# Optimization experiments

Hardware: AMD Instinct MI355X
Metric: run time of the kernel (lower is better)

Reference implementation:

```python
import jax, jax.numpy as jnp
import numpy as np

N_NODES = 50000
N_EDGES = 800000
IN_CH = 128
HID = 64
OUT_CH = 40


def _sage_conv(x, src, dst, W_l, b_l, W_r):
    # PyG SAGEConv (mean aggr): out = lin_l(mean_{j in N(i)} x_j) + lin_r(x_i)
    msgs = x[src]                                                # [E, d]
    summed = jax.ops.segment_sum(msgs, dst, num_segments=N_NODES)
    counts = jax.ops.segment_sum(jnp.ones((src.shape[0],), x.dtype), dst,
                                 num_segments=N_NODES)
    mean = summed / jnp.maximum(counts, 1.0)[:, None]            # [N, d]
    return mean @ W_l.T + b_l + x @ W_r.T


def setup_inputs() -> dict:
    key = jax.random.key(0)
    ks = jax.random.split(key, 8)
    x = jax.random.normal(ks[0], (N_NODES, IN_CH), dtype=jnp.float32)
    edge_index = jax.random.randint(ks[1], (2, N_EDGES), 0, N_NODES, dtype=jnp.int64)
    s1 = 1.0 / np.sqrt(IN_CH)
    s2 = 1.0 / np.sqrt(HID)
    W1_l = jax.random.uniform(ks[2], (HID, IN_CH), jnp.float32, -s1, s1)
    W1_r = jax.random.uniform(ks[3], (HID, IN_CH), jnp.float32, -s1, s1)
    b1 = jax.random.uniform(ks[4], (HID,), jnp.float32, -s1, s1)
    W2_l = jax.random.uniform(ks[5], (OUT_CH, HID), jnp.float32, -s2, s2)
    W2_r = jax.random.uniform(ks[6], (OUT_CH, HID), jnp.float32, -s2, s2)
    b2 = jax.random.uniform(ks[7], (OUT_CH,), jnp.float32, -s2, s2)
    return {"x": x, "edge_index": edge_index, "W1_l": W1_l, "b1": b1,
            "W1_r": W1_r, "W2_l": W2_l, "b2": b2, "W2_r": W2_r}


def reference(x, edge_index, W1_l, b1, W1_r, W2_l, b2, W2_r):
    src, dst = edge_index[0], edge_index[1]
    h = _sage_conv(x, src, dst, W1_l, b1, W1_r)
    h = jax.nn.relu(h)                       # dropout is identity in eval
    h = _sage_conv(h, src, dst, W2_l, b2, W2_r)
    return jax.nn.log_softmax(h, axis=-1)
```

## Files before the change

kernel.cpp:

```cpp
#include <hip/hip_runtime.h>

#define N_NODES 50000
#define N_EDGES 800000
#define IN_CH 128
#define HID 64
#define OUT_CH 40
#define BSHIFT 7
#define BNODES 128
#define NBUCKETS 391
#define NBLK 256
#define EPB 3125
#define NSEG (NBUCKETS * NBLK)
#define SCHUNK 1024
#define NSCANA ((NSEG + SCHUNK - 1) / SCHUNK)
#define MAXB 4096
#define NXBLK 782


typedef __attribute__((ext_vector_type(8))) short short8v;
typedef __attribute__((ext_vector_type(4))) float float4v;

__device__ __forceinline__ unsigned f2bf_u(float f) {
  unsigned u = __float_as_uint(f);
  return (u + 0x7FFF + ((u >> 16) & 1)) >> 16;
}
__device__ __forceinline__ ushort f2bf(float f) { return (ushort)f2bf_u(f); }
__device__ __forceinline__ float bf2f(ushort u) {
  return __uint_as_float(((unsigned)u) << 16);
}
__device__ __forceinline__ float bflo(unsigned u) {
  return __uint_as_float(u << 16);
}
__device__ __forceinline__ float bfhi(unsigned u) {
  return __uint_as_float(u & 0xFFFF0000u);
}

__device__ __forceinline__ uint4 pack8(const float* p) {
  float4 a = *reinterpret_cast<const float4*>(p);
  float4 b = *reinterpret_cast<const float4*>(p + 4);
  uint4 r;
  r.x = f2bf_u(a.x) | (f2bf_u(a.y) << 16);
  r.y = f2bf_u(a.z) | (f2bf_u(a.w) << 16);
  r.z = f2bf_u(b.x) | (f2bf_u(b.y) << 16);
  r.w = f2bf_u(b.z) | (f2bf_u(b.w) << 16);
  return r;
}

__global__ __launch_bounds__(256) void histX_kernel(
    const int* __restrict__ dst, int* __restrict__ blkcnt,
    const float* __restrict__ x, const float* __restrict__ W1l,
    const float* __restrict__ W1r, const float* __restrict__ b1,
    ushort* __restrict__ xwl, float* __restrict__ xwr) {
  __shared__ int h[NBUCKETS];
  __shared__ ushort sWl[64 * 128];
  __shared__ ushort sWr[64 * 128];
  __shared__ ushort sx[64 * 128];
  __shared__ float sb[64];

  if (blockIdx.x < NBLK) {
    for (int i = threadIdx.x; i < NBUCKETS; i += 256) h[i] = 0;
    __syncthreads();
    int blk = blockIdx.x;
    int e0 = blk * EPB, e1 = min(e0 + EPB, N_EDGES);
    for (int e = e0 + threadIdx.x; e < e1; e += 256)
      atomicAdd(&h[dst[e] >> BSHIFT], 1);
    __syncthreads();
    for (int i = threadIdx.x; i < NBUCKETS; i += 256)
      blkcnt[(i << 8) | blk] = h[i];
    return;
  }

  int nblk = (blockIdx.x - NBLK) * 64;
  for (int q = threadIdx.x; q < 1024; q += 256) {
    int row = q >> 4, c8 = (q & 15) << 3;
    int boff = row * 256 + (((c8 << 1)) ^ ((row & 15) << 4));
    int n = nblk + row;
    uint4 p = make_uint4(0, 0, 0, 0);
    if (n < N_NODES) p = pack8(x + (size_t)n * IN_CH + c8);
    *reinterpret_cast<uint4*>((char*)sx + boff) = p;
  }
  for (int q = threadIdx.x; q < 1024; q += 256) {
    int row = q >> 4, c8 = (q & 15) << 3;
    int boff = row * 256 + (((c8 << 1)) ^ ((row & 15) << 4));
    *reinterpret_cast<uint4*>((char*)sWl + boff) =
        pack8(W1l + row * IN_CH + c8);
    *reinterpret_cast<uint4*>((char*)sWr + boff) =
        pack8(W1r + row * IN_CH + c8);
  }
  if (threadIdx.x < 64) sb[threadIdx.x] = b1[threadIdx.x];
  __syncthreads();

  int wave = threadIdx.x >> 6, lane = threadIdx.x & 63;
  int nloc = lane & 15, g = lane >> 4;

  float4v accl[4], accr[4];
#pragma unroll
  for (int m = 0; m < 4; ++m) {
    accl[m] = (float4v){0.f, 0.f, 0.f, 0.f};
    accr[m] = (float4v){0.f, 0.f, 0.f, 0.f};
  }

  int xrow = wave * 16 + nloc;
#pragma unroll
  for (int kt = 0; kt < 4; ++kt) {
    int cb = kt * 64 + g * 16;
    short8v bx = *reinterpret_cast<const short8v*>(
        (char*)sx + xrow * 256 + (cb ^ ((xrow & 15) << 4)));
#pragma unroll
    for (int m = 0; m < 4; ++m) {
      int wrow = m * 16 + nloc;
      int so = wrow * 256 + (cb ^ ((wrow & 15) << 4));
      short8v al = *reinterpret_cast<const short8v*>((char*)sWl + so);
      short8v ar = *reinterpret_cast<const short8v*>((char*)sWr + so);
      accl[m] = __builtin_amdgcn_mfma_f32_16x16x32_bf16(al, bx, accl[m], 0, 0, 0);
      accr[m] = __builtin_amdgcn_mfma_f32_16x16x32_bf16(ar, bx, accr[m], 0, 0, 0);
    }
  }

  int n = nblk + wave * 16 + nloc;
  if (n < N_NODES) {
#pragma unroll
    for (int m = 0; m < 4; ++m) {
      int h0 = m * 16 + g * 4;
      uint2 pl;
      pl.x = f2bf_u(accl[m][0]) | (f2bf_u(accl[m][1]) << 16);
      pl.y = f2bf_u(accl[m][2]) | (f2bf_u(accl[m][3]) << 16);
      *reinterpret_cast<uint2*>(xwl + (size_t)n * HID + h0) = pl;
      float4 vr;
      vr.x = accr[m][0] + sb[h0 + 0];
      vr.y = accr[m][1] + sb[h0 + 1];
      vr.z = accr[m][2] + sb[h0 + 2];
      vr.w = accr[m][3] + sb[h0 + 3];
      *reinterpret_cast<float4*>(xwr + (size_t)n * HID + h0) = vr;
    }
  }
}

__global__ __launch_bounds__(256) void scanA_kernel(
    const int* __restrict__ blkcnt, int* __restrict__ segoff,
    int* __restrict__ asum) {
  __shared__ int s[256];
  int t = threadIdx.x;
  int idx0 = blockIdx.x * SCHUNK + t * 4;
  int v[4], tot = 0;
#pragma unroll
  for (int j = 0; j < 4; ++j) {
    int i = idx0 + j;
    v[j] = (i < NSEG) ? blkcnt[i] : 0;
    tot += v[j];
  }
  s[t] = tot;
  __syncthreads();
  for (int o = 1; o < 256; o <<= 1) {
    int u = (t >= o) ? s[t - o] : 0;
    __syncthreads();
    s[t] += u;
    __syncthreads();
  }
  int pre = s[t] - tot;
#pragma unroll
  for (int j = 0; j < 4; ++j) {
    int i = idx0 + j;
    if (i < NSEG) segoff[i] = pre;
    pre += v[j];
  }
  if (t == 255) asum[blockIdx.x] = s[255];
}

__global__ __launch_bounds__(256) void scanB_kernel(int* __restrict__ asum) {
  __shared__ int s[256];
  int t = threadIdx.x;
  int v = (t < NSCANA) ? asum[t] : 0;
  s[t] = v;
  __syncthreads();
  for (int o = 1; o < 256; o <<= 1) {
    int u = (t >= o) ? s[t - o] : 0;
    __syncthreads();
    s[t] += u;
    __syncthreads();
  }
  if (t < NSCANA) asum[t] = s[t] - v;
}

__global__ __launch_bounds__(256) void scanC_kernel(int* __restrict__ segoff,
                                                    const int* __restrict__ asum) {
  int add = asum[blockIdx.x];
  int idx0 = blockIdx.x * SCHUNK + threadIdx.x * 4;
#pragma unroll
  for (int j = 0; j < 4; ++j) {
    int i = idx0 + j;
    if (i < NSEG) segoff[i] += add;
  }
}

__global__ __launch_bounds__(256) void placeB_kernel(
    const int* __restrict__ src, const int* __restrict__ dst,
    const int* __restrict__ segoff, unsigned* __restrict__ pairbuf) {
  __shared__ int cur[NBUCKETS];
  int blk = blockIdx.x;
  for (int b = threadIdx.x; b < NBUCKETS; b += 256)
    cur[b] = segoff[(b << 8) | blk];
  __syncthreads();
  int e0 = blk * EPB, e1 = min(e0 + EPB, N_EDGES);
  for (int e = e0 + threadIdx.x; e < e1; e += 256) {
    int d = dst[e];
    int pos = atomicAdd(&cur[d >> BSHIFT], 1);
    pairbuf[pos] = ((unsigned)src[e] << BSHIFT) | (unsigned)(d & (BNODES - 1));
  }
}

__global__ __launch_bounds__(256) void placeC_kernel(
    const unsigned* __restrict__ pairbuf, const int* __restrict__ segoff,
    int* __restrict__ cnt, int* __restrict__ off, int* __restrict__ csr) {
  __shared__ int lcnt[BNODES];
  __shared__ int woff[BNODES];
  __shared__ int lcur[BNODES];
  __shared__ int sscan[256];
  __shared__ int slot[MAXB];
  int b = blockIdx.x;
  int start = segoff[b << 8];
  int end = (b == NBUCKETS - 1) ? N_EDGES : segoff[(b + 1) << 8];
  int n0 = b << BSHIFT;
  int nn = min(BNODES, N_NODES - n0);
  int len = end - start;
  for (int i = threadIdx.x; i < nn; i += 256) {
    lcnt[i] = 0;
    lcur[i] = 0;
  }
  __syncthreads();
  for (int p = start + threadIdx.x; p < end; p += 256)
    atomicAdd(&lcnt[pairbuf[p] & (BNODES - 1)], 1);
  __syncthreads();
  int v = (threadIdx.x < nn) ? lcnt[threadIdx.x] : 0;
  sscan[threadIdx.x] = v;
  __syncthreads();
  for (int o = 1; o < 256; o <<= 1) {
    int t2 = (threadIdx.x >= o) ? sscan[threadIdx.x - o] : 0;
    __syncthreads();
    sscan[threadIdx.x] += t2;
    __syncthreads();
  }
  if (threadIdx.x < nn) {
    woff[threadIdx.x] = sscan[threadIdx.x] - v;
    cnt[n0 + threadIdx.x] = v;
    off[n0 + threadIdx.x] = start + sscan[threadIdx.x] - v;
  }
  __syncthreads();
  if (len <= MAXB) {
    for (int p = start + threadIdx.x; p < end; p += 256) {
      unsigned e = pairbuf[p];
      int local = (int)(e & (BNODES - 1));
      int pos = woff[local] + atomicAdd(&lcur[local], 1);
      slot[pos] = (int)(e >> BSHIFT);
    }
    __syncthreads();
    for (int p = threadIdx.x; p < len; p += 256) csr[start + p] = slot[p];
  } else {
    for (int p = start + threadIdx.x; p < end; p += 256) {
      unsigned e = pairbuf[p];
      int local = (int)(e & (BNODES - 1));
      int pos = woff[local] + atomicAdd(&lcur[local], 1);
      csr[start + pos] = (int)(e >> BSHIFT);
    }
  }
}

__global__ __launch_bounds__(256) void agg1_kernel(
    const ushort* __restrict__ xwl, const float* __restrict__ xwr,
    const int* __restrict__ cnt, const int* __restrict__ off,
    const int* __restrict__ csr, float* __restrict__ h1) {
  int wave = threadIdx.x >> 6, lane = threadIdx.x & 63;
  int n = blockIdx.x * 4 + wave;
  if (n >= N_NODES) return;

  int deg = cnt[n], base = off[n];
  int half = lane >> 5;
  int cp = lane & 31;
  float ax = 0.f, ay = 0.f;

  if (deg > 0) {
    int k = 0;
    for (; k + 16 <= deg; k += 16) {
      int e[8];
#pragma unroll
      for (int j = 0; j < 8; ++j) e[j] = csr[base + k + 2 * j + half];
      unsigned u[8];
#pragma unroll
      for (int j = 0; j < 8; ++j)
        u[j] = *reinterpret_cast<const unsigned*>(xwl + (size_t)e[j] * HID +
                                                  2 * cp);
#pragma unroll
      for (int j = 0; j < 8; ++j) {
        ax += bflo(u[j]);
        ay += bfhi(u[j]);
      }
    }
    if (k + 8 <= deg) {
      int e[4];
#pragma unroll
      for (int j = 0; j < 4; ++j) e[j] = csr[base + k + 2 * j + half];
      unsigned u[4];
#pragma unroll
      for (int j = 0; j < 4; ++j)
        u[j] = *reinterpret_cast<const unsigned*>(xwl + (size_t)e[j] * HID +
                                                  2 * cp);
#pragma unroll
      for (int j = 0; j < 4; ++j) {
        ax += bflo(u[j]);
        ay += bfhi(u[j]);
      }
      k += 8;
    }
    if (k < deg) {
#pragma unroll
      for (int j = 0; j < 4; ++j) {
        int idx = k + 2 * j + half;
        bool valid = idx < deg;
        int e = csr[base + (valid ? idx : 0)];
        unsigned u =
            *reinterpret_cast<const unsigned*>(xwl + (size_t)e * HID + 2 * cp);
        if (valid) {
          ax += bflo(u);
          ay += bfhi(u);
        }
      }
    }
    ax += __shfl_xor(ax, 32);
    ay += __shfl_xor(ay, 32);
  }

  float inv = 1.0f / fmaxf((float)deg, 1.0f);
  const float2 s =
      *reinterpret_cast<const float2*>(xwr + (size_t)n * HID + 2 * cp);
  float2 h;
  h.x = fmaxf(ax * inv + s.x, 0.f);
  h.y = fmaxf(ay * inv + s.y, 0.f);
  if (half == 0)
    *reinterpret_cast<float2*>(h1 + (size_t)n * HID + 2 * cp) = h;
}

__global__ __launch_bounds__(256) void xform2_kernel(
    const float* __restrict__ h1, const float* __restrict__ W2l,
    const float* __restrict__ W2r, const float* __restrict__ b2,
    ushort* __restrict__ hw2, float* __restrict__ self2) {
  __shared__ unsigned sWl[HID / 2][OUT_CH + 1];
  __shared__ unsigned sWr[HID / 2][OUT_CH + 1];
  __shared__ float sh[32][HID];
  for (int i = threadIdx.x; i < OUT_CH * (HID / 2); i += 256) {
    int o = i >> 5, c2 = i & 31;
    float a = W2l[o * HID + 2 * c2], b = W2l[o * HID + 2 * c2 + 1];
    sWl[c2][o] = (unsigned)f2bf(a) | ((unsigned)f2bf(b) << 16);
    float c = W2r[o * HID + 2 * c2], d = W2r[o * HID + 2 * c2 + 1];
    sWr[c2][o] = (unsigned)f2bf(c) | ((unsigned)f2bf(d) << 16);
  }
  int nblk = blockIdx.x * 32;
  for (int s = threadIdx.x; s < 32 * (HID / 4); s += 256) {
    int node = s >> 4, c4 = s & 15;
    int n = nblk + node;
    float4 v = make_float4(0.f, 0.f, 0.f, 0.f);
    if (n < N_NODES)
      v = *reinterpret_cast<const float4*>(h1 + (size_t)n * HID + c4 * 4);
    *reinterpret_cast<float4*>(&sh[node][c4 * 4]) = v;
  }
  __syncthreads();

  int wave = threadIdx.x >> 6, lane = threadIdx.x & 63;
  int n0 = nblk + wave * 8;
  if (n0 >= N_NODES || lane >= OUT_CH) return;
  float bias = b2[lane];

  float accl[8], accr[8];
#pragma unroll
  for (int i = 0; i < 8; ++i) {
    accl[i] = 0.f;
    accr[i] = bias;
  }
  const int nb = wave * 8;
  int nvalid = min(8, N_NODES - n0);
  for (int c = 0; c < HID; c += 4) {
    unsigned ul0 = sWl[(c >> 1) + 0][lane], ul1 = sWl[(c >> 1) + 1][lane];
    unsigned ur0 = sWr[(c >> 1) + 0][lane], ur1 = sWr[(c >> 1) + 1][lane];
    float wl0 = bflo(ul0), wl1 = bfhi(ul0), wl2 = bflo(ul1), wl3 = bfhi(ul1);
    float wr0 = bflo(ur0), wr1 = bfhi(ur0), wr2 = bflo(ur1), wr3 = bfhi(ur1);
#pragma unroll
    for (int i = 0; i < 8; ++i) {
      const float4 hv = *reinterpret_cast<const float4*>(&sh[nb + i][c]);
      accl[i] = fmaf(hv.x, wl0, accl[i]);
      accr[i] = fmaf(hv.x, wr0, accr[i]);
      accl[i] = fmaf(hv.y, wl1, accl[i]);
      accr[i] = fmaf(hv.y, wr1, accr[i]);
      accl[i] = fmaf(hv.z, wl2, accl[i]);
      accr[i] = fmaf(hv.z, wr2, accr[i]);
      accl[i] = fmaf(hv.w, wl3, accl[i]);
      accr[i] = fmaf(hv.w, wr3, accr[i]);
    }
  }
  for (int i = 0; i < nvalid; ++i) {
    hw2[(size_t)(n0 + i) * OUT_CH + lane] = f2bf(accl[i]);
    self2[(size_t)(n0 + i) * OUT_CH + lane] = accr[i];
  }
}

__global__ __launch_bounds__(256) void agg2_kernel(
    const ushort* __restrict__ hw2, const float* __restrict__ self2,
    const int* __restrict__ cnt, const int* __restrict__ off,
    const int* __restrict__ csr, float* __restrict__ out) {
  int wave = threadIdx.x >> 6, lane = threadIdx.x & 63;
  int n = blockIdx.x * 4 + wave;
  if (n >= N_NODES) return;

  int deg = cnt[n], base = off[n];
  float logit = -1e30f;
  if (lane < OUT_CH) {
    float acc = 0.f;
    int k = 0;
    for (; k + 16 <= deg; k += 16) {
      int e[16];
#pragma unroll
      for (int j = 0; j < 16; ++j) e[j] = csr[base + k + j];
      float v[16];
#pragma unroll
      for (int j = 0; j < 16; ++j)
        v[j] = bf2f(hw2[(size_t)e[j] * OUT_CH + lane]);
#pragma unroll
      for (int j = 0; j < 16; ++j) acc += v[j];
    }
    if (k + 8 <= deg) {
      int e[8];
#pragma unroll
      for (int j = 0; j < 8; ++j) e[j] = csr[base + k + j];
      float v[8];
#pragma unroll
      for (int j = 0; j < 8; ++j)
        v[j] = bf2f(hw2[(size_t)e[j] * OUT_CH + lane]);
#pragma unroll
      for (int j = 0; j < 8; ++j) acc += v[j];
      k += 8;
    }
    if (k < deg) {
#pragma unroll
      for (int i = 0; i < 8; ++i) {
        int kk = k + i;
        int s_ = csr[base + (kk < deg ? kk : k)];
        float v = bf2f(hw2[(size_t)s_ * OUT_CH + lane]);
        if (kk < deg) acc += v;
      }
    }
    logit = acc / fmaxf((float)deg, 1.0f) + self2[(size_t)n * OUT_CH + lane];
  }
  float m = logit;
  for (int o = 32; o; o >>= 1) m = fmaxf(m, __shfl_xor(m, o));
  float e = (lane < OUT_CH) ? expf(logit - m) : 0.f;
  float ssum = e;
  for (int o = 32; o; o >>= 1) ssum += __shfl_xor(ssum, o);
  float lse = logf(ssum);
  if (lane < OUT_CH) out[(size_t)n * OUT_CH + lane] = logit - m - lse;
}

extern "C" void kernel_launch(void* const* d_in, const int* in_sizes, int n_in,
                              void* d_out, int out_size, void* d_ws, size_t ws_size,
                              hipStream_t stream) {
  const float* x   = (const float*)d_in[0];
  const int*   ei  = (const int*)d_in[1];
  const float* W1l = (const float*)d_in[2];
  const float* b1  = (const float*)d_in[3];
  const float* W1r = (const float*)d_in[4];
  const float* W2l = (const float*)d_in[5];
  const float* b2  = (const float*)d_in[6];
  const float* W2r = (const float*)d_in[7];
  float* out = (float*)d_out;

  const int* src = ei;
  const int* dst = ei + N_EDGES;

  float* xwr   = (float*)d_ws;
  float* self2 = xwr + (size_t)N_NODES * HID;
  float* h1    = self2 + (size_t)N_NODES * OUT_CH;
  ushort* xwl  = (ushort*)(h1 + (size_t)N_NODES * HID);
  ushort* hw2  = xwl + (size_t)N_NODES * HID;
  unsigned* pairbuf = (unsigned*)(hw2 + (size_t)N_NODES * OUT_CH);
  int* blkcnt = (int*)(pairbuf + N_EDGES);
  int* segoff = blkcnt + NSEG;
  int* asum   = segoff + NSEG;
  int* cnt    = asum + 256;
  int* off    = cnt + N_NODES;
  int* csr    = off + N_NODES;

  histX_kernel<<<NBLK + NXBLK, 256, 0, stream>>>(dst, blkcnt, x, W1l, W1r, b1,
                                                 xwl, xwr);
  scanA_kernel<<<NSCANA, 256, 0, stream>>>(blkcnt, segoff, asum);
  scanB_kernel<<<1, 256, 0, stream>>>(asum);
  scanC_kernel<<<NSCANA, 256, 0, stream>>>(segoff, asum);
  placeB_kernel<<<NBLK, 256, 0, stream>>>(src, dst, segoff, pairbuf);
  placeC_kernel<<<NBUCKETS, 256, 0, stream>>>(pairbuf, segoff, cnt, off, csr);

  agg1_kernel<<<(N_NODES + 3) / 4, 256, 0, stream>>>(xwl, xwr, cnt, off, csr,
                                                     h1);
  xform2_kernel<<<(N_NODES + 31) / 32, 256, 0, stream>>>(h1, W2l, W2r, b2, hw2,
                                                         self2);
  agg2_kernel<<<(N_NODES + 3) / 4, 256, 0, stream>>>(hw2, self2, cnt, off, csr,
                                                     out);
}
```

Before: 121.4 us.

## Fold scan fixup into placement kernels and pack edges across lanes in agg2

Drops the scanC kernel launch and instead adds the per-chunk scan offset (asum) directly where placeB and placeC read segoff. This saves one launch and one full read-modify-write pass over the segment offsets. The agg2 kernel is also reworked so each wave processes three edges at once: every lane loads a bf16 pair of channels, the three partial sums are combined with shuffles, and log-softmax is done with float2 loads and stores. This uses 60 of 64 lanes instead of 40 and cuts the number of dependent gather iterations, at the cost of extra shuffles and predicated loads.

```diff
diff --git a/kernel.cpp b/kernel.cpp
--- a/kernel.cpp
+++ b/kernel.cpp
@@ -182,24 +182,16 @@
   if (t < NSCANA) asum[t] = s[t] - v;
 }
 
-__global__ __launch_bounds__(256) void scanC_kernel(int* __restrict__ segoff,
-                                                    const int* __restrict__ asum) {
-  int add = asum[blockIdx.x];
-  int idx0 = blockIdx.x * SCHUNK + threadIdx.x * 4;
-#pragma unroll
-  for (int j = 0; j < 4; ++j) {
-    int i = idx0 + j;
-    if (i < NSEG) segoff[i] += add;
-  }
-}
-
 __global__ __launch_bounds__(256) void placeB_kernel(
     const int* __restrict__ src, const int* __restrict__ dst,
-    const int* __restrict__ segoff, unsigned* __restrict__ pairbuf) {
+    const int* __restrict__ segoff, const int* __restrict__ asum,
+    unsigned* __restrict__ pairbuf) {
   __shared__ int cur[NBUCKETS];
   int blk = blockIdx.x;
-  for (int b = threadIdx.x; b < NBUCKETS; b += 256)
-    cur[b] = segoff[(b << 8) | blk];
+  for (int b = threadIdx.x; b < NBUCKETS; b += 256) {
+    int i = (b << 8) | blk;
+    cur[b] = segoff[i] + asum[i >> 10];
+  }
   __syncthreads();
   int e0 = blk * EPB, e1 = min(e0 + EPB, N_EDGES);
   for (int e = e0 + threadIdx.x; e < e1; e += 256) {
@@ -211,15 +203,21 @@
 
 __global__ __launch_bounds__(256) void placeC_kernel(
     const unsigned* __restrict__ pairbuf, const int* __restrict__ segoff,
-    int* __restrict__ cnt, int* __restrict__ off, int* __restrict__ csr) {
+    const int* __restrict__ asum, int* __restrict__ cnt,
+    int* __restrict__ off, int* __restrict__ csr) {
   __shared__ int lcnt[BNODES];
   __shared__ int woff[BNODES];
   __shared__ int lcur[BNODES];
   __shared__ int sscan[256];
   __shared__ int slot[MAXB];
   int b = blockIdx.x;
-  int start = segoff[b << 8];
-  int end = (b == NBUCKETS - 1) ? N_EDGES : segoff[(b + 1) << 8];
+  int i0 = b << 8;
+  int start = segoff[i0] + asum[i0 >> 10];
+  int end = N_EDGES;
+  if (b != NBUCKETS - 1) {
+    int i1 = (b + 1) << 8;
+    end = segoff[i1] + asum[i1 >> 10];
+  }
   int n0 = b << BSHIFT;
   int nn = min(BNODES, N_NODES - n0);
   int len = end - start;
@@ -410,51 +408,49 @@
   if (n >= N_NODES) return;
 
   int deg = cnt[n], base = off[n];
-  float logit = -1e30f;
-  if (lane < OUT_CH) {
-    float acc = 0.f;
-    int k = 0;
-    for (; k + 16 <= deg; k += 16) {
-      int e[16];
-#pragma unroll
-      for (int j = 0; j < 16; ++j) e[j] = csr[base + k + j];
-      float v[16];
-#pragma unroll
-      for (int j = 0; j < 16; ++j)
-        v[j] = bf2f(hw2[(size_t)e[j] * OUT_CH + lane]);
-#pragma unroll
-      for (int j = 0; j < 16; ++j) acc += v[j];
-    }
-    if (k + 8 <= deg) {
-      int e[8];
-#pragma unroll
-      for (int j = 0; j < 8; ++j) e[j] = csr[base + k + j];
-      float v[8];
-#pragma unroll
-      for (int j = 0; j < 8; ++j)
-        v[j] = bf2f(hw2[(size_t)e[j] * OUT_CH + lane]);
-#pragma unroll
-      for (int j = 0; j < 8; ++j) acc += v[j];
-      k += 8;
-    }
-    if (k < deg) {
-#pragma unroll
-      for (int i = 0; i < 8; ++i) {
-        int kk = k + i;
-        int s_ = csr[base + (kk < deg ? kk : k)];
-        float v = bf2f(hw2[(size_t)s_ * OUT_CH + lane]);
-        if (kk < deg) acc += v;
+  int eslot = lane / 20;
+  int cp = lane - eslot * 20;
+  bool act = eslot < 3;
+  float ax = 0.f, ay = 0.f;
+
+  for (int k = 0; k < deg; k += 12) {
+#pragma unroll
+    for (int j = 0; j < 4; ++j) {
+      int idx = k + 3 * j + eslot;
+      bool valid = act && idx < deg;
+      int e = csr[base + (valid ? idx : 0)];
+      unsigned u = *reinterpret_cast<const unsigned*>(
+          hw2 + (size_t)e * OUT_CH + 2 * cp);
+      if (valid) {
+        ax += bflo(u);
+        ay += bfhi(u);
       }
     }
-    logit = acc / fmaxf((float)deg, 1.0f) + self2[(size_t)n * OUT_CH + lane];
-  }
-  float m = logit;
+  }
+  float t1 = __shfl(ax, cp + 20), t2 = __shfl(ax, cp + 40);
+  float t3 = __shfl(ay, cp + 20), t4 = __shfl(ay, cp + 40);
+  ax += t1 + t2;
+  ay += t3 + t4;
+
+  float lx = -1e30f, ly = -1e30f;
+  if (lane < 20) {
+    float inv = 1.0f / fmaxf((float)deg, 1.0f);
+    const float2 s =
+        *reinterpret_cast<const float2*>(self2 + (size_t)n * OUT_CH + 2 * cp);
+    lx = ax * inv + s.x;
+    ly = ay * inv + s.y;
+  }
+  float m = fmaxf(lx, ly);
   for (int o = 32; o; o >>= 1) m = fmaxf(m, __shfl_xor(m, o));
-  float e = (lane < OUT_CH) ? expf(logit - m) : 0.f;
-  float ssum = e;
+  float ssum = (lane < 20) ? (expf(lx - m) + expf(ly - m)) : 0.f;
   for (int o = 32; o; o >>= 1) ssum += __shfl_xor(ssum, o);
   float lse = logf(ssum);
-  if (lane < OUT_CH) out[(size_t)n * OUT_CH + lane] = logit - m - lse;
+  if (lane < 20) {
+    float2 r;
+    r.x = lx - m - lse;
+    r.y = ly - m - lse;
+    *reinterpret_cast<float2*>(out + (size_t)n * OUT_CH + 2 * cp) = r;
+  }
 }
 
 extern "C" void kernel_launch(void* const* d_in, const int* in_sizes, int n_in,
@@ -490,9 +486,9 @@
                                                  xwl, xwr);
   scanA_kernel<<<NSCANA, 256, 0, stream>>>(blkcnt, segoff, asum);
   scanB_kernel<<<1, 256, 0, stream>>>(asum);
-  scanC_kernel<<<NSCANA, 256, 0, stream>>>(segoff, asum);
-  placeB_kernel<<<NBLK, 256, 0, stream>>>(src, dst, segoff, pairbuf);
-  placeC_kernel<<<NBUCKETS, 256, 0, stream>>>(pairbuf, segoff, cnt, off, csr);
+  placeB_kernel<<<NBLK, 256, 0, stream>>>(src, dst, segoff, asum, pairbuf);
+  placeC_kernel<<<NBUCKETS, 256, 0, stream>>>(pairbuf, segoff, asum, cnt, off,
+                                              csr);
 
   agg1_kernel<<<(N_NODES + 3) / 4, 256, 0, stream>>>(xwl, xwr, cnt, off, csr,
                                                      h1);
```

Measured after the change: 133.3 us. 1.1x slower.
